# Kernel tuning notes

Hardware: AMD Instinct MI355X
Metric: run time of the kernel (lower is better)

Reference implementation:

```python
import jax, jax.numpy as jnp
import numpy as np

COMMITMENT_COST = 0.25
NUM_EMBEDDINGS = 8192
EMBED_DIM = 64


def setup_inputs() -> dict:
    key = jax.random.key(0)
    k1, k2 = jax.random.split(key)
    inputs = jax.random.normal(k1, (16, 32, 32, EMBED_DIM), dtype=jnp.float32)
    # nn.init.uniform_(-1/K, 1/K)
    codebook = jax.random.uniform(
        k2, (NUM_EMBEDDINGS, EMBED_DIM), dtype=jnp.float32,
        minval=-1.0 / NUM_EMBEDDINGS, maxval=1.0 / NUM_EMBEDDINGS)
    return {"inputs": inputs, "codebook": codebook}


def reference(inputs, codebook):
    D = codebook.shape[-1]
    flat = inputs.reshape(-1, D)  # [N, D]
    # Squared euclidean distances (same argmin as torch.cdist).
    d2 = (jnp.sum(flat * flat, axis=1, keepdims=True)
          - 2.0 * flat @ codebook.T
          + jnp.sum(codebook * codebook, axis=1))  # [N, K]
    idx = jnp.argmin(d2, axis=1)  # [N]
    # one-hot @ codebook == direct gather
    quantized = codebook[idx].reshape(inputs.shape)
    sg = jax.lax.stop_gradient
    e_latent = (sg(quantized) - inputs) ** 2
    q_latent = (quantized - sg(inputs)) ** 2
    loss = q_latent + COMMITMENT_COST * e_latent
    quantized_st = inputs + sg(quantized - inputs)  # straight-through
    return (loss, quantized_st)
```

## Files before the change

### kernel.cpp

```cpp
#include <hip/hip_runtime.h>
#include <float.h>

#define NROWS 16384
#define KC 8192
#define DIM 64
#define BM 128
#define BN 128
#define KSPLIT 4
#define CODES_PER_BLOCK (KC / KSPLIT)
#define ITERS (CODES_PER_BLOCK / BN)

typedef __attribute__((ext_vector_type(8))) short bf16x8;
typedef __attribute__((ext_vector_type(4))) float f32x4;

#define WS_CB16 0
#define WS_NORM 1048576
#define WS_PV   (WS_NORM + 32768)
#define WS_PI   (WS_PV + 262144)

__device__ inline unsigned short f2bf(float f) {
    union { float f; unsigned u; } v; v.f = f;
    unsigned u = v.u;
    unsigned r = u + 0x7FFFu + ((u >> 16) & 1u);
    return (unsigned short)(r >> 16);
}

__global__ __launch_bounds__(256) void vq_norms(const float* __restrict__ cb,
                                                float* __restrict__ norms) {
    int k = blockIdx.x * 256 + threadIdx.x;
    const float4* c4 = (const float4*)(cb + (size_t)k * DIM);
    float4 acc = make_float4(0.f, 0.f, 0.f, 0.f);
#pragma unroll
    for (int i = 0; i < DIM / 4; ++i) {
        float4 v = c4[i];
        acc.x = fmaf(v.x, v.x, acc.x);
        acc.y = fmaf(v.y, v.y, acc.y);
        acc.z = fmaf(v.z, v.z, acc.z);
        acc.w = fmaf(v.w, v.w, acc.w);
    }
    norms[k] = (acc.x + acc.y) + (acc.z + acc.w);
}

__global__ __launch_bounds__(256) void vq_cvt(const float* __restrict__ cb,
                                              unsigned short* __restrict__ cb16) {
    int t = blockIdx.x * 256 + threadIdx.x;
    const float4* s = (const float4*)cb + (size_t)t * 2;
    float4 a = s[0], b = s[1];
    bf16x8 o;
    o[0] = (short)f2bf(a.x); o[1] = (short)f2bf(a.y);
    o[2] = (short)f2bf(a.z); o[3] = (short)f2bf(a.w);
    o[4] = (short)f2bf(b.x); o[5] = (short)f2bf(b.y);
    o[6] = (short)f2bf(b.z); o[7] = (short)f2bf(b.w);
    ((bf16x8*)cb16)[t] = o;
}

__global__ __launch_bounds__(256, 2) void vq_main(
        const float* __restrict__ x, const unsigned short* __restrict__ cb16,
        const float* __restrict__ cbnorm,
        float* __restrict__ pv, int* __restrict__ pi) {
    __shared__ __attribute__((aligned(16))) char smem[32768];
    __shared__ __attribute__((aligned(16))) float nrmLds[CODES_PER_BLOCK];

    const int tid = threadIdx.x;
    const int lane = tid & 63;
    const int wave = tid >> 6;
    const int waveM = wave >> 1, waveN = wave & 1;
    const int quad = lane >> 4, c15 = lane & 15;

    const int bx = blockIdx.x;
    const int rowTile = bx & (NROWS / BM - 1);
    const int split = bx >> 7;
    const int splitBase = split * CODES_PER_BLOCK;
    const size_t rowBase = (size_t)rowTile * BM;

    {
        const float4* s = (const float4*)(cbnorm + splitBase) + tid * 2;
        float4* d = (float4*)nrmLds + tid * 2;
        d[0] = s[0]; d[1] = s[1];
    }

    {
        bf16x8* xb = (bf16x8*)smem;
#pragma unroll
        for (int i = 0; i < 4; ++i) {
            int p = tid + 256 * i;
            int r = p >> 3, cp = p & 7;
            int c = cp ^ (r & 7);
            const float4* src = (const float4*)(x + (rowBase + r) * DIM + c * 8);
            float4 a = src[0], b = src[1];
            bf16x8 o;
            o[0] = (short)f2bf(-2.f * a.x); o[1] = (short)f2bf(-2.f * a.y);
            o[2] = (short)f2bf(-2.f * a.z); o[3] = (short)f2bf(-2.f * a.w);
            o[4] = (short)f2bf(-2.f * b.x); o[5] = (short)f2bf(-2.f * b.y);
            o[6] = (short)f2bf(-2.f * b.z); o[7] = (short)f2bf(-2.f * b.w);
            xb[p] = o;
        }
    }
    __syncthreads();

    bf16x8 afr[4][2];
    {
        const bf16x8* lds16 = (const bf16x8*)smem;
#pragma unroll
        for (int fm = 0; fm < 4; ++fm) {
            int r = waveM * 64 + fm * 16 + c15;
#pragma unroll
            for (int kk = 0; kk < 2; ++kk) {
                int cch = kk * 4 + quad;
                afr[fm][kk] = lds16[r * 8 + (cch ^ (r & 7))];
            }
        }
    }
    __syncthreads();

    unsigned srcOff[4], ldsOff[4];
#pragma unroll
    for (int j = 0; j < 4; ++j) {
        int p = (wave * 4 + j) * 64 + lane;
        int q = (p & ~7) | ((p & 7) ^ ((p >> 3) & 7));
        srcOff[j] = (unsigned)q * 16u;
        ldsOff[j] = (unsigned)(wave * 4 + j) * 1024u;
    }

    const char* gcb = (const char*)cb16 + (size_t)splitBase * DIM * 2;

    f32x4 acc[4][4];
    float minv[4][4];
    int mini[4][4];
#pragma unroll
    for (int a = 0; a < 4; ++a)
#pragma unroll
        for (int b = 0; b < 4; ++b) { minv[a][b] = FLT_MAX; mini[a][b] = 0; }
    const f32x4 Z = {0.f, 0.f, 0.f, 0.f};

    {
        const char* g0 = gcb;
#pragma unroll
        for (int j = 0; j < 4; ++j)
            __builtin_amdgcn_global_load_lds(
                (const __attribute__((address_space(1))) void*)(g0 + srcOff[j]),
                (__attribute__((address_space(3))) void*)(smem + ldsOff[j]),
                16, 0, 0);
    }
    __syncthreads();

    for (int iter = 0; iter < ITERS; ++iter) {
        const int buf = iter & 1;
        if (iter + 1 < ITERS) {
            const char* gn = gcb + (size_t)(iter + 1) * BN * DIM * 2;
            char* lb = smem + (buf ^ 1) * 16384;
#pragma unroll
            for (int j = 0; j < 4; ++j)
                __builtin_amdgcn_global_load_lds(
                    (const __attribute__((address_space(1))) void*)(gn + srcOff[j]),
                    (__attribute__((address_space(3))) void*)(lb + ldsOff[j]),
                    16, 0, 0);
        }

        const bf16x8* B16 = (const bf16x8*)(smem + buf * 16384);
        bf16x8 bfr[4][2];
#pragma unroll
        for (int fn = 0; fn < 4; ++fn) {
            int rB = waveN * 64 + fn * 16 + c15;
#pragma unroll
            for (int kk = 0; kk < 2; ++kk) {
                int cch = kk * 4 + quad;
                bfr[fn][kk] = B16[rB * 8 + (cch ^ (rB & 7))];
            }
        }

#pragma unroll
        for (int fm = 0; fm < 4; ++fm)
#pragma unroll
            for (int fn = 0; fn < 4; ++fn) {
                f32x4 t = __builtin_amdgcn_mfma_f32_16x16x32_bf16(
                    afr[fm][0], bfr[fn][0], Z, 0, 0, 0);
                acc[fm][fn] = __builtin_amdgcn_mfma_f32_16x16x32_bf16(
                    afr[fm][1], bfr[fn][1], t, 0, 0, 0);
            }

#pragma unroll
        for (int fn = 0; fn < 4; ++fn) {
            float nrm = nrmLds[iter * BN + waveN * 64 + fn * 16 + c15];
            int slot = iter * 4 + fn;
#pragma unroll
            for (int fm = 0; fm < 4; ++fm) {
#pragma unroll
                for (int rg = 0; rg < 4; ++rg) {
                    float g = acc[fm][fn][rg] + nrm;
                    bool lt = (g < minv[fm][rg]);
                    mini[fm][rg] = lt ? slot : mini[fm][rg];
                    minv[fm][rg] = fminf(minv[fm][rg], g);
                }
            }
        }
        __syncthreads();
    }

    float* redv = (float*)smem;
    int* redi = (int*)(smem + 16384);
#pragma unroll
    for (int fm = 0; fm < 4; ++fm)
#pragma unroll
        for (int rg = 0; rg < 4; ++rg) {
            int r = waveM * 64 + fm * 16 + quad * 4 + rg;
            int slot = waveN * 16 + c15;
            int pk = mini[fm][rg];
            redv[r * 32 + slot] = minv[fm][rg];
            redi[r * 32 + slot] = splitBase + waveN * 64 +
                                  (pk >> 2) * 128 + (pk & 3) * 16 + c15;
        }
    __syncthreads();
    if (tid < BM) {
        float bv = redv[tid * 32];
        int bi = redi[tid * 32];
        for (int j = 1; j < 32; ++j) {
            float v = redv[tid * 32 + j];
            int ii = redi[tid * 32 + j];
            if (v < bv || (v == bv && ii < bi)) { bv = v; bi = ii; }
        }
        pv[(rowBase + tid) * KSPLIT + split] = bv;
        pi[(rowBase + tid) * KSPLIT + split] = bi;
    }
}

__global__ __launch_bounds__(256) void vq_out(
        const float* __restrict__ x, const float* __restrict__ cb,
        const float* __restrict__ pv, const int* __restrict__ pi,
        float* __restrict__ out_loss, float* __restrict__ out_q) {
    __shared__ int idxs[16];
    const int tid = threadIdx.x;
    const size_t row0 = (size_t)blockIdx.x * 16;
    if (tid < 16) {
        size_t r = row0 + tid;
        float bv = pv[r * KSPLIT];
        int bi = pi[r * KSPLIT];
        for (int s = 1; s < KSPLIT; ++s) {
            float v = pv[r * KSPLIT + s];
            int ii = pi[r * KSPLIT + s];
            if (v < bv || (v == bv && ii < bi)) { bv = v; bi = ii; }
        }
        idxs[tid] = bi;
    }
    __syncthreads();
    const int r = tid >> 4;
    const int d4 = tid & 15;
    const int code = idxs[r];
    float4 q4 = ((const float4*)(cb + (size_t)code * DIM))[d4];
    float4 x4 = ((const float4*)(x + (row0 + r) * DIM))[d4];
    float4 l4;
    l4.x = 1.25f * (q4.x - x4.x) * (q4.x - x4.x);
    l4.y = 1.25f * (q4.y - x4.y) * (q4.y - x4.y);
    l4.z = 1.25f * (q4.z - x4.z) * (q4.z - x4.z);
    l4.w = 1.25f * (q4.w - x4.w) * (q4.w - x4.w);
    ((float4*)out_loss)[(row0 + r) * 16 + d4] = l4;
    ((float4*)out_q)[(row0 + r) * 16 + d4] = q4;
}

extern "C" void kernel_launch(void* const* d_in, const int* in_sizes, int n_in,
                              void* d_out, int out_size, void* d_ws, size_t ws_size,
                              hipStream_t stream) {
    const float* x = (const float*)d_in[0];
    const float* cb = (const float*)d_in[1];
    char* ws = (char*)d_ws;
    unsigned short* cb16 = (unsigned short*)(ws + WS_CB16);
    float* norms = (float*)(ws + WS_NORM);
    float* pvb = (float*)(ws + WS_PV);
    int* pib = (int*)(ws + WS_PI);

    float* out_loss = (float*)d_out;
    float* out_q = out_loss + (size_t)NROWS * DIM;

    vq_norms<<<KC / 256, 256, 0, stream>>>(cb, norms);
    vq_cvt<<<(KC * DIM / 8) / 256, 256, 0, stream>>>(cb, cb16);
    vq_main<<<(NROWS / BM) * KSPLIT, 256, 0, stream>>>(x, cb16, norms, pvb, pib);
    vq_out<<<NROWS / 16, 256, 0, stream>>>(x, cb, pvb, pib, out_loss, out_q);
}
```

Measured before the change: 99.27 us.

## Fuse prep kernels, pack argmin keys, raise k-split, reduce via atomicMin

Merges the norm and bf16 conversion kernels into one prep kernel that also initializes a per-row global min buffer. The main kernel now uses KSPLIT=16 and loads its whole 512-code slice into LDS at once, dropping the double-buffered loop. It folds the codebook norm into the MFMA accumulator init and packs the code index into the low 13 mantissa bits, so a single fminf tracks value and index together. Partial results are combined with a shuffle reduction and then atomicMin on an order-preserving unsigned encoding, replacing the LDS reduction and the partial-result arrays. Dropping 13 mantissa bits coarsens distance comparisons and can change argmin on near ties, and the larger split adds atomic traffic and more blocks.

```diff
diff --git a/kernel.cpp b/kernel.cpp
--- a/kernel.cpp
+++ b/kernel.cpp
@@ -5,18 +5,16 @@
 #define KC 8192
 #define DIM 64
 #define BM 128
-#define BN 128
-#define KSPLIT 4
-#define CODES_PER_BLOCK (KC / KSPLIT)
-#define ITERS (CODES_PER_BLOCK / BN)
+#define KSPLIT 16
+#define CPB (KC / KSPLIT)
+#define NSUB (CPB / 128)
 
 typedef __attribute__((ext_vector_type(8))) short bf16x8;
 typedef __attribute__((ext_vector_type(4))) float f32x4;
 
 #define WS_CB16 0
-#define WS_NORM 1048576
-#define WS_PV   (WS_NORM + 32768)
-#define WS_PI   (WS_PV + 262144)
+#define WS_NORM (KC * DIM * 2)
+#define WS_GMIN (WS_NORM + KC * 4)
 
 __device__ inline unsigned short f2bf(float f) {
     union { float f; unsigned u; } v; v.f = f;
@@ -24,42 +22,38 @@
     unsigned r = u + 0x7FFFu + ((u >> 16) & 1u);
     return (unsigned short)(r >> 16);
 }
-
-__global__ __launch_bounds__(256) void vq_norms(const float* __restrict__ cb,
-                                                float* __restrict__ norms) {
-    int k = blockIdx.x * 256 + threadIdx.x;
-    const float4* c4 = (const float4*)(cb + (size_t)k * DIM);
-    float4 acc = make_float4(0.f, 0.f, 0.f, 0.f);
-#pragma unroll
-    for (int i = 0; i < DIM / 4; ++i) {
-        float4 v = c4[i];
-        acc.x = fmaf(v.x, v.x, acc.x);
-        acc.y = fmaf(v.y, v.y, acc.y);
-        acc.z = fmaf(v.z, v.z, acc.z);
-        acc.w = fmaf(v.w, v.w, acc.w);
-    }
-    norms[k] = (acc.x + acc.y) + (acc.z + acc.w);
-}
-
-__global__ __launch_bounds__(256) void vq_cvt(const float* __restrict__ cb,
-                                              unsigned short* __restrict__ cb16) {
-    int t = blockIdx.x * 256 + threadIdx.x;
-    const float4* s = (const float4*)cb + (size_t)t * 2;
-    float4 a = s[0], b = s[1];
-    bf16x8 o;
-    o[0] = (short)f2bf(a.x); o[1] = (short)f2bf(a.y);
-    o[2] = (short)f2bf(a.z); o[3] = (short)f2bf(a.w);
-    o[4] = (short)f2bf(b.x); o[5] = (short)f2bf(b.y);
-    o[6] = (short)f2bf(b.z); o[7] = (short)f2bf(b.w);
-    ((bf16x8*)cb16)[t] = o;
+__device__ inline unsigned asu(float f) { union { float f; unsigned u; } v; v.f = f; return v.u; }
+__device__ inline float asf(unsigned u) { union { float f; unsigned u; } v; v.u = u; return v.f; }
+
+__global__ __launch_bounds__(256) void vq_prep(const float* __restrict__ cb,
+        unsigned short* __restrict__ cb16, float* __restrict__ norms,
+        unsigned* __restrict__ gmin) {
+    const int g = blockIdx.x * 256 + threadIdx.x;
+    const int c = g >> 2, q = g & 3;
+    const float4* s = (const float4*)cb + (size_t)c * 16 + q * 4;
+    float4 a = s[0], b = s[1], d = s[2], e = s[3];
+    float p = 0.f;
+    p = fmaf(a.x, a.x, p); p = fmaf(a.y, a.y, p); p = fmaf(a.z, a.z, p); p = fmaf(a.w, a.w, p);
+    p = fmaf(b.x, b.x, p); p = fmaf(b.y, b.y, p); p = fmaf(b.z, b.z, p); p = fmaf(b.w, b.w, p);
+    p = fmaf(d.x, d.x, p); p = fmaf(d.y, d.y, p); p = fmaf(d.z, d.z, p); p = fmaf(d.w, d.w, p);
+    p = fmaf(e.x, e.x, p); p = fmaf(e.y, e.y, p); p = fmaf(e.z, e.z, p); p = fmaf(e.w, e.w, p);
+    bf16x8 o0, o1;
+    o0[0] = (short)f2bf(a.x); o0[1] = (short)f2bf(a.y); o0[2] = (short)f2bf(a.z); o0[3] = (short)f2bf(a.w);
+    o0[4] = (short)f2bf(b.x); o0[5] = (short)f2bf(b.y); o0[6] = (short)f2bf(b.z); o0[7] = (short)f2bf(b.w);
+    o1[0] = (short)f2bf(d.x); o1[1] = (short)f2bf(d.y); o1[2] = (short)f2bf(d.z); o1[3] = (short)f2bf(d.w);
+    o1[4] = (short)f2bf(e.x); o1[5] = (short)f2bf(e.y); o1[6] = (short)f2bf(e.z); o1[7] = (short)f2bf(e.w);
+    bf16x8* dst = (bf16x8*)cb16 + (size_t)c * 8 + q * 2;
+    dst[0] = o0; dst[1] = o1;
+    p += __shfl_xor(p, 1);
+    p += __shfl_xor(p, 2);
+    if (q == 0) norms[c] = p;
+    if (g < NROWS) gmin[g] = 0xFFFFFFFFu;
 }
 
 __global__ __launch_bounds__(256, 2) void vq_main(
         const float* __restrict__ x, const unsigned short* __restrict__ cb16,
-        const float* __restrict__ cbnorm,
-        float* __restrict__ pv, int* __restrict__ pi) {
-    __shared__ __attribute__((aligned(16))) char smem[32768];
-    __shared__ __attribute__((aligned(16))) float nrmLds[CODES_PER_BLOCK];
+        const float* __restrict__ cbnorm, unsigned* __restrict__ gmin) {
+    __shared__ __attribute__((aligned(16))) char smem[65536];
 
     const int tid = threadIdx.x;
     const int lane = tid & 63;
@@ -67,180 +61,123 @@
     const int waveM = wave >> 1, waveN = wave & 1;
     const int quad = lane >> 4, c15 = lane & 15;
 
-    const int bx = blockIdx.x;
-    const int rowTile = bx & (NROWS / BM - 1);
-    const int split = bx >> 7;
-    const int splitBase = split * CODES_PER_BLOCK;
+    const int rowTile = blockIdx.x & 127;
+    const int split = blockIdx.x >> 7;
+    const int splitBase = split * CPB;
     const size_t rowBase = (size_t)rowTile * BM;
 
-    {
-        const float4* s = (const float4*)(cbnorm + splitBase) + tid * 2;
-        float4* d = (float4*)nrmLds + tid * 2;
-        d[0] = s[0]; d[1] = s[1];
-    }
-
-    {
-        bf16x8* xb = (bf16x8*)smem;
-#pragma unroll
-        for (int i = 0; i < 4; ++i) {
-            int p = tid + 256 * i;
-            int r = p >> 3, cp = p & 7;
-            int c = cp ^ (r & 7);
-            const float4* src = (const float4*)(x + (rowBase + r) * DIM + c * 8);
-            float4 a = src[0], b = src[1];
+    const char* gcb = (const char*)cb16 + (size_t)splitBase * DIM * 2;
+#pragma unroll
+    for (int j = 0; j < 16; ++j) {
+        int p = j * 256 + tid;
+        int q = (p & ~7) | ((p & 7) ^ ((p >> 3) & 7));
+        __builtin_amdgcn_global_load_lds(
+            (const __attribute__((address_space(1))) void*)(gcb + (size_t)q * 16),
+            (__attribute__((address_space(3))) void*)(smem + (size_t)(j * 256 + wave * 64) * 16),
+            16, 0, 0);
+    }
+
+    bf16x8 afr[4][2];
+#pragma unroll
+    for (int fm = 0; fm < 4; ++fm) {
+        const float* xr = x + (rowBase + waveM * 64 + fm * 16 + c15) * DIM;
+#pragma unroll
+        for (int kk = 0; kk < 2; ++kk) {
+            const float4* s4 = (const float4*)(xr + kk * 32 + quad * 8);
+            float4 a = s4[0], b = s4[1];
             bf16x8 o;
             o[0] = (short)f2bf(-2.f * a.x); o[1] = (short)f2bf(-2.f * a.y);
             o[2] = (short)f2bf(-2.f * a.z); o[3] = (short)f2bf(-2.f * a.w);
             o[4] = (short)f2bf(-2.f * b.x); o[5] = (short)f2bf(-2.f * b.y);
             o[6] = (short)f2bf(-2.f * b.z); o[7] = (short)f2bf(-2.f * b.w);
-            xb[p] = o;
+            afr[fm][kk] = o;
         }
     }
+
+    float nrmv[NSUB][4];
+#pragma unroll
+    for (int st = 0; st < NSUB; ++st)
+#pragma unroll
+        for (int fn = 0; fn < 4; ++fn)
+            nrmv[st][fn] = cbnorm[splitBase + st * 128 + waveN * 64 + fn * 16 + c15];
+
     __syncthreads();
 
-    bf16x8 afr[4][2];
-    {
-        const bf16x8* lds16 = (const bf16x8*)smem;
-#pragma unroll
-        for (int fm = 0; fm < 4; ++fm) {
-            int r = waveM * 64 + fm * 16 + c15;
-#pragma unroll
-            for (int kk = 0; kk < 2; ++kk) {
-                int cch = kk * 4 + quad;
-                afr[fm][kk] = lds16[r * 8 + (cch ^ (r & 7))];
-            }
-        }
-    }
-    __syncthreads();
-
-    unsigned srcOff[4], ldsOff[4];
-#pragma unroll
-    for (int j = 0; j < 4; ++j) {
-        int p = (wave * 4 + j) * 64 + lane;
-        int q = (p & ~7) | ((p & 7) ^ ((p >> 3) & 7));
-        srcOff[j] = (unsigned)q * 16u;
-        ldsOff[j] = (unsigned)(wave * 4 + j) * 1024u;
-    }
-
-    const char* gcb = (const char*)cb16 + (size_t)splitBase * DIM * 2;
-
-    f32x4 acc[4][4];
-    float minv[4][4];
-    int mini[4][4];
+    const unsigned laneSlotBase = (unsigned)(splitBase + waveN * 64 + c15);
+    float key[4][4];
 #pragma unroll
     for (int a = 0; a < 4; ++a)
 #pragma unroll
-        for (int b = 0; b < 4; ++b) { minv[a][b] = FLT_MAX; mini[a][b] = 0; }
-    const f32x4 Z = {0.f, 0.f, 0.f, 0.f};
-
-    {
-        const char* g0 = gcb;
-#pragma unroll
-        for (int j = 0; j < 4; ++j)
-            __builtin_amdgcn_global_load_lds(
-                (const __attribute__((address_space(1))) void*)(g0 + srcOff[j]),
-                (__attribute__((address_space(3))) void*)(smem + ldsOff[j]),
-                16, 0, 0);
-    }
-    __syncthreads();
-
-    for (int iter = 0; iter < ITERS; ++iter) {
-        const int buf = iter & 1;
-        if (iter + 1 < ITERS) {
-            const char* gn = gcb + (size_t)(iter + 1) * BN * DIM * 2;
-            char* lb = smem + (buf ^ 1) * 16384;
-#pragma unroll
-            for (int j = 0; j < 4; ++j)
-                __builtin_amdgcn_global_load_lds(
-                    (const __attribute__((address_space(1))) void*)(gn + srcOff[j]),
-                    (__attribute__((address_space(3))) void*)(lb + ldsOff[j]),
-                    16, 0, 0);
-        }
-
-        const bf16x8* B16 = (const bf16x8*)(smem + buf * 16384);
+        for (int b = 0; b < 4; ++b) key[a][b] = FLT_MAX;
+
+    const bf16x8* B16 = (const bf16x8*)smem;
+
+#pragma unroll
+    for (int st = 0; st < NSUB; ++st) {
         bf16x8 bfr[4][2];
 #pragma unroll
         for (int fn = 0; fn < 4; ++fn) {
-            int rB = waveN * 64 + fn * 16 + c15;
+            int rB = st * 128 + waveN * 64 + fn * 16 + c15;
 #pragma unroll
             for (int kk = 0; kk < 2; ++kk) {
                 int cch = kk * 4 + quad;
                 bfr[fn][kk] = B16[rB * 8 + (cch ^ (rB & 7))];
             }
         }
-
 #pragma unroll
         for (int fm = 0; fm < 4; ++fm)
 #pragma unroll
             for (int fn = 0; fn < 4; ++fn) {
+                f32x4 ci;
+                ci[0] = nrmv[st][fn]; ci[1] = nrmv[st][fn];
+                ci[2] = nrmv[st][fn]; ci[3] = nrmv[st][fn];
                 f32x4 t = __builtin_amdgcn_mfma_f32_16x16x32_bf16(
-                    afr[fm][0], bfr[fn][0], Z, 0, 0, 0);
-                acc[fm][fn] = __builtin_amdgcn_mfma_f32_16x16x32_bf16(
+                    afr[fm][0], bfr[fn][0], ci, 0, 0, 0);
+                f32x4 g = __builtin_amdgcn_mfma_f32_16x16x32_bf16(
                     afr[fm][1], bfr[fn][1], t, 0, 0, 0);
-            }
-
-#pragma unroll
-        for (int fn = 0; fn < 4; ++fn) {
-            float nrm = nrmLds[iter * BN + waveN * 64 + fn * 16 + c15];
-            int slot = iter * 4 + fn;
-#pragma unroll
-            for (int fm = 0; fm < 4; ++fm) {
+                const unsigned slot = laneSlotBase + (unsigned)(st * 128 + fn * 16);
 #pragma unroll
                 for (int rg = 0; rg < 4; ++rg) {
-                    float g = acc[fm][fn][rg] + nrm;
-                    bool lt = (g < minv[fm][rg]);
-                    mini[fm][rg] = lt ? slot : mini[fm][rg];
-                    minv[fm][rg] = fminf(minv[fm][rg], g);
+                    unsigned u = (asu(g[rg]) & 0xFFFFE000u) | slot;
+                    key[fm][rg] = fminf(key[fm][rg], asf(u));
                 }
             }
+    }
+
+#pragma unroll
+    for (int fm = 0; fm < 4; ++fm)
+#pragma unroll
+        for (int rg = 0; rg < 4; ++rg) {
+            float k = key[fm][rg];
+            k = fminf(k, __shfl_xor(k, 1));
+            k = fminf(k, __shfl_xor(k, 2));
+            k = fminf(k, __shfl_xor(k, 4));
+            k = fminf(k, __shfl_xor(k, 8));
+            key[fm][rg] = k;
         }
-        __syncthreads();
-    }
-
-    float* redv = (float*)smem;
-    int* redi = (int*)(smem + 16384);
-#pragma unroll
-    for (int fm = 0; fm < 4; ++fm)
-#pragma unroll
-        for (int rg = 0; rg < 4; ++rg) {
-            int r = waveM * 64 + fm * 16 + quad * 4 + rg;
-            int slot = waveN * 16 + c15;
-            int pk = mini[fm][rg];
-            redv[r * 32 + slot] = minv[fm][rg];
-            redi[r * 32 + slot] = splitBase + waveN * 64 +
-                                  (pk >> 2) * 128 + (pk & 3) * 16 + c15;
-        }
-    __syncthreads();
-    if (tid < BM) {
-        float bv = redv[tid * 32];
-        int bi = redi[tid * 32];
-        for (int j = 1; j < 32; ++j) {
-            float v = redv[tid * 32 + j];
-            int ii = redi[tid * 32 + j];
-            if (v < bv || (v == bv && ii < bi)) { bv = v; bi = ii; }
-        }
-        pv[(rowBase + tid) * KSPLIT + split] = bv;
-        pi[(rowBase + tid) * KSPLIT + split] = bi;
+    if (c15 == 0) {
+#pragma unroll
+        for (int fm = 0; fm < 4; ++fm)
+#pragma unroll
+            for (int rg = 0; rg < 4; ++rg) {
+                unsigned u = asu(key[fm][rg]);
+                unsigned m = (u & 0x80000000u) ? ~u : (u | 0x80000000u);
+                atomicMin(&gmin[rowBase + waveM * 64 + fm * 16 + quad * 4 + rg], m);
+            }
     }
 }
 
 __global__ __launch_bounds__(256) void vq_out(
         const float* __restrict__ x, const float* __restrict__ cb,
-        const float* __restrict__ pv, const int* __restrict__ pi,
+        const unsigned* __restrict__ gmin,
         float* __restrict__ out_loss, float* __restrict__ out_q) {
     __shared__ int idxs[16];
     const int tid = threadIdx.x;
     const size_t row0 = (size_t)blockIdx.x * 16;
     if (tid < 16) {
-        size_t r = row0 + tid;
-        float bv = pv[r * KSPLIT];
-        int bi = pi[r * KSPLIT];
-        for (int s = 1; s < KSPLIT; ++s) {
-            float v = pv[r * KSPLIT + s];
-            int ii = pi[r * KSPLIT + s];
-            if (v < bv || (v == bv && ii < bi)) { bv = v; bi = ii; }
-        }
-        idxs[tid] = bi;
+        unsigned u = gmin[row0 + tid];
+        unsigned b = (u & 0x80000000u) ? (u ^ 0x80000000u) : ~u;
+        idxs[tid] = (int)(b & 8191u);
     }
     __syncthreads();
     const int r = tid >> 4;
@@ -265,14 +202,12 @@
     char* ws = (char*)d_ws;
     unsigned short* cb16 = (unsigned short*)(ws + WS_CB16);
     float* norms = (float*)(ws + WS_NORM);
-    float* pvb = (float*)(ws + WS_PV);
-    int* pib = (int*)(ws + WS_PI);
+    unsigned* gmin = (unsigned*)(ws + WS_GMIN);
 
     float* out_loss = (float*)d_out;
     float* out_q = out_loss + (size_t)NROWS * DIM;
 
-    vq_norms<<<KC / 256, 256, 0, stream>>>(cb, norms);
-    vq_cvt<<<(KC * DIM / 8) / 256, 256, 0, stream>>>(cb, cb16);
-    vq_main<<<(NROWS / BM) * KSPLIT, 256, 0, stream>>>(x, cb16, norms, pvb, pib);
-    vq_out<<<NROWS / 16, 256, 0, stream>>>(x, cb, pvb, pib, out_loss, out_q);
-}
+    vq_prep<<<128, 256, 0, stream>>>(cb, cb16, norms, gmin);
+    vq_main<<<(NROWS / BM) * KSPLIT, 256, 0, stream>>>(x, cb16, norms, gmin);
+    vq_out<<<NROWS / 16, 256, 0, stream>>>(x, cb, gmin, out_loss, out_q);
+}
```

After: 98.38 us. No clear change (-0.9%).
